# Kernel optimization log

Hardware: AMD Instinct MI355X
Metric: run time of the kernel (lower is better)

## Reference

```python
import jax, jax.numpy as jnp
import numpy as np

N = 100000      # nodes
E = 3200000     # edges (before self loops)
IN = 128        # in_channels
H = 8           # heads
C = 16          # out_channels per head
NEG_SLOPE = 0.2


def setup_inputs() -> dict:
    key = jax.random.key(0)
    k1, k2, k3, k4, k5, k6 = jax.random.split(key, 6)
    x = jax.random.normal(k1, (N, IN), dtype=jnp.float32)
    edge_index = jax.random.randint(k2, (2, E), 0, N, dtype=jnp.int32)
    # GATConv params: lin weight [IN, H*C], att_src/att_dst [H, C], bias [H*C]
    W = jax.random.normal(k3, (IN, H * C), dtype=jnp.float32) / np.float32(np.sqrt(IN))
    att_src = jax.random.normal(k4, (H, C), dtype=jnp.float32) / np.float32(np.sqrt(C))
    att_dst = jax.random.normal(k5, (H, C), dtype=jnp.float32) / np.float32(np.sqrt(C))
    bias = jax.random.normal(k6, (H * C,), dtype=jnp.float32) * 0.01
    return {"x": x, "edge_index": edge_index, "W": W,
            "att_src": att_src, "att_dst": att_dst, "bias": bias}


def reference(x, edge_index, W, att_src, att_dst, bias):
    n = x.shape[0]
    h = (x @ W).reshape(n, H, C)                      # [N, H, C]
    # add self loops (PyG default add_self_loops=True)
    loop = jnp.arange(n, dtype=edge_index.dtype)
    src = jnp.concatenate([edge_index[0], loop])      # [E+N] message sources j
    dst = jnp.concatenate([edge_index[1], loop])      # [E+N] targets i
    # per-node attention logits
    a_src = jnp.einsum('nhc,hc->nh', h, att_src)      # [N, H]
    a_dst = jnp.einsum('nhc,hc->nh', h, att_dst)      # [N, H]
    alpha = jax.nn.leaky_relu(a_src[src] + a_dst[dst], NEG_SLOPE)  # [E+N, H]
    # segment softmax over edges grouped by destination node
    amax = jax.lax.stop_gradient(jax.ops.segment_max(alpha, dst, num_segments=n))
    ex = jnp.exp(alpha - amax[dst])
    denom = jax.ops.segment_sum(ex, dst, num_segments=n)           # [N, H]
    w = ex / (denom[dst] + 1e-16)                                  # [E+N, H]
    msg = h[src] * w[:, :, None]                                   # [E+N, H, C]
    out = jax.ops.segment_sum(msg, dst, num_segments=n)            # [N, H, C]
    return out.reshape(n, H * C) + bias
```

## Files before the change

### kernel.cpp

```cpp
#include <hip/hip_runtime.h>
#include <hip/hip_bf16.h>

#define H 8
#define C 16
#define HC 128
#define NEG 0.2f
#define XS_S 132

#define BKT_SH 8
#define BKT_MSK 255
#define MAXB 1024
#define EPB 4096

__device__ __forceinline__ float lrelu(float x) { return fmaxf(x, NEG * x); }

__device__ __forceinline__ unsigned pack_bf16(float a, float b) {
    union { __hip_bfloat16 h; unsigned short u; } ua, ub;
    ua.h = __float2bfloat16(a);
    ub.h = __float2bfloat16(b);
    return (unsigned)ua.u | ((unsigned)ub.u << 16);
}
__device__ __forceinline__ float bf_lo(unsigned d) { return __uint_as_float(d << 16); }
__device__ __forceinline__ float bf_hi(unsigned d) { return __uint_as_float(d & 0xffff0000u); }

__global__ void __launch_bounds__(256) k1_gemm(const float* __restrict__ x,
                                               const float* __restrict__ W,
                                               const float* __restrict__ att_src,
                                               const float* __restrict__ att_dst,
                                               unsigned* __restrict__ h16,
                                               float* __restrict__ a_src,
                                               float* __restrict__ a_dst, int N) {
    __shared__ float xs[64 * XS_S];
    const int n0 = blockIdx.x * 64;
    const int t = threadIdx.x;
#pragma unroll
    for (int i = 0; i < 8; ++i) {
        int id = t + 256 * i;
        int r = id >> 5, kq = id & 31;
        int n = n0 + r;
        float4 v = (n < N) ? ((const float4*)x)[(size_t)n * 32 + kq]
                           : make_float4(0.f, 0.f, 0.f, 0.f);
        *(float4*)&xs[r * XS_S + kq * 4] = v;
    }
    __syncthreads();
    const int cg = t & 31;
    const int r0 = (t >> 5) * 8;
    float acc[8][4];
#pragma unroll
    for (int i = 0; i < 8; ++i)
#pragma unroll
        for (int j = 0; j < 4; ++j) acc[i][j] = 0.f;

#pragma unroll 4
    for (int k = 0; k < HC; ++k) {
        const float4 wv = ((const float4*)W)[k * 32 + cg];
        float wr[4] = {wv.x, wv.y, wv.z, wv.w};
#pragma unroll
        for (int i = 0; i < 8; ++i) {
            float xv = xs[(r0 + i) * XS_S + k];
#pragma unroll
            for (int j = 0; j < 4; ++j) acc[i][j] += xv * wr[j];
        }
    }
    const int fhd = cg >> 2;
    const int cq  = cg & 3;
#pragma unroll
    for (int i = 0; i < 8; ++i) {
        int n = n0 + r0 + i;
        if (n < N) {
            uint2 dv = make_uint2(pack_bf16(acc[i][0], acc[i][1]),
                                  pack_bf16(acc[i][2], acc[i][3]));
            *(uint2*)&h16[(size_t)n * 64 + cg * 2] = dv;
        }
        float ps = 0.f, pd = 0.f;
#pragma unroll
        for (int jj = 0; jj < 4; ++jj) {
            float hv = acc[i][jj];
            ps += hv * att_src[fhd * C + cq * 4 + jj];
            pd += hv * att_dst[fhd * C + cq * 4 + jj];
        }
        ps += __shfl_xor(ps, 1, 4); pd += __shfl_xor(pd, 1, 4);
        ps += __shfl_xor(ps, 2, 4); pd += __shfl_xor(pd, 2, 4);
        if (cq == 0 && n < N) {
            a_src[(unsigned)n * 8u + fhd] = ps;
            a_dst[(unsigned)n * 8u + fhd] = pd;
        }
    }
}


__global__ void __launch_bounds__(256) kh_bucket(const int* __restrict__ ei,
                                                 int* __restrict__ bcount,
                                                 int E, int B) {
    __shared__ int hist[MAXB];
    const int t = threadIdx.x;
    for (int i = t; i < B; i += 256) hist[i] = 0;
    __syncthreads();
    const int e0 = blockIdx.x * EPB;
    const int nE = min(EPB, E - e0);
    for (int i = t; i < nE; i += 256)
        atomicAdd(&hist[ei[E + e0 + i] >> BKT_SH], 1);
    __syncthreads();
    for (int i = t; i < B; i += 256)
        if (hist[i]) atomicAdd(&bcount[i], hist[i]);
}

__global__ void __launch_bounds__(1024) kscan_b(const int* __restrict__ bcount,
                                                int* __restrict__ bptr,
                                                int* __restrict__ gcursor,
                                                int* __restrict__ rowptr,
                                                int N, int B, int E) {
    __shared__ int s[MAXB];
    const int t = threadIdx.x;
    s[t] = (t < B) ? bcount[t] : 0;
    __syncthreads();
    for (int off = 1; off < MAXB; off <<= 1) {
        int v = (t >= off) ? s[t - off] : 0;
        __syncthreads();
        s[t] += v;
        __syncthreads();
    }
    if (t < B) {
        bptr[t + 1] = s[t];
        gcursor[t] = s[t] - bcount[t];
    }
    if (t == 0) { bptr[0] = 0; rowptr[N] = E; }
}

__global__ void __launch_bounds__(256) kb_bin(const int* __restrict__ ei,
                                              int* __restrict__ gcursor,
                                              unsigned* __restrict__ pairs,
                                              int E, int B) {
    __shared__ int hist[MAXB];
    __shared__ int lbase[MAXB];
    const int t = threadIdx.x;
    const int e0 = blockIdx.x * EPB;
    const int nE = min(EPB, E - e0);
    for (int i = t; i < B; i += 256) hist[i] = 0;
    __syncthreads();
    for (int i = t; i < nE; i += 256)
        atomicAdd(&hist[ei[E + e0 + i] >> BKT_SH], 1);
    __syncthreads();
    for (int i = t; i < B; i += 256) {
        int h = hist[i];
        if (h) lbase[i] = atomicAdd(&gcursor[i], h);
    }
    __syncthreads();
    for (int i = t; i < nE; i += 256) {
        int dst = ei[E + e0 + i];
        int src = ei[e0 + i];
        int b = dst >> BKT_SH;
        int pos = atomicAdd(&lbase[b], 1);
        pairs[pos] = (unsigned)src | ((unsigned)(dst & BKT_MSK) << 18);
    }
}

__global__ void __launch_bounds__(256) kb_final(const unsigned* __restrict__ pairs,
                                                const int* __restrict__ bptr,
                                                int* __restrict__ rowptr,
                                                int* __restrict__ col, int N) {
    __shared__ int cnt[256];
    __shared__ int incl[256];
    __shared__ int lcur[256];
    const int b = blockIdx.x;
    const int t = threadIdx.x;
    const int n0 = b << BKT_SH;
    const int jbeg = bptr[b], jend = bptr[b + 1];
    cnt[t] = 0;
    __syncthreads();
    for (int j = jbeg + t; j < jend; j += 256)
        atomicAdd(&cnt[pairs[j] >> 18], 1);
    __syncthreads();
    incl[t] = cnt[t];
    __syncthreads();
    for (int off = 1; off < 256; off <<= 1) {
        int v = (t >= off) ? incl[t - off] : 0;
        __syncthreads();
        incl[t] += v;
        __syncthreads();
    }
    const int base = jbeg + incl[t] - cnt[t];
    if (n0 + t < N) rowptr[n0 + t] = base;
    lcur[t] = base;
    __syncthreads();
    for (int j = jbeg + t; j < jend; j += 256) {
        unsigned v = pairs[j];
        int pos = atomicAdd(&lcur[v >> 18], 1);
        col[pos] = (int)(v & 0x3FFFF);
    }
}

__global__ void __launch_bounds__(256) k_pull(const int* __restrict__ rowptr,
                                              const int* __restrict__ col,
                                              const unsigned* __restrict__ h16,
                                              const float* __restrict__ a_src,
                                              const float* __restrict__ a_dst,
                                              const float* __restrict__ bias,
                                              float* __restrict__ out, int N) {
    const int node = blockIdx.x * 4 + (threadIdx.x >> 6);
    if (node >= N) return;
    const int t = threadIdx.x & 63;
    const int hd = t >> 3;
    const int hh = t & 7;
    const int bidx = hd * 4;

    const float adst_own = a_dst[(unsigned)node * 8u + (unsigned)hd];
    const float adst_hh  = a_dst[(unsigned)node * 8u + (unsigned)hh];
    const float wself = __expf(lrelu(a_src[(unsigned)node * 8u + (unsigned)hd] + adst_own));
    unsigned dself = h16[(unsigned)node * 64u + (unsigned)t];
    float a0 = bf_lo(dself) * wself, a1 = bf_hi(dself) * wself;
    float b0 = 0.f, b1 = 0.f, c0 = 0.f, c1 = 0.f, e0 = 0.f, e1 = 0.f;
    float sA = wself, sB = 0.f, sC = 0.f, sD = 0.f;

    const int beg = rowptr[node], end = rowptr[node + 1];
    int j = beg;
    for (; j + 8 <= end; j += 8) {
        int n0_ = col[j],     n1 = col[j + 1], n2 = col[j + 2], n3 = col[j + 3];
        int n4  = col[j + 4], n5 = col[j + 5], n6 = col[j + 6], n7 = col[j + 7];
        int nP = col[j + (t >> 3)];
        float wme = __expf(lrelu(a_src[(unsigned)nP * 8u + (unsigned)hh] + adst_hh));
        int wi = __float_as_int(wme);
        float w0 = __int_as_float(__builtin_amdgcn_ds_bpermute(bidx,       wi));
        float w1 = __int_as_float(__builtin_amdgcn_ds_bpermute(bidx + 32,  wi));
        float w2 = __int_as_float(__builtin_amdgcn_ds_bpermute(bidx + 64,  wi));
        float w3 = __int_as_float(__builtin_amdgcn_ds_bpermute(bidx + 96,  wi));
        float w4 = __int_as_float(__builtin_amdgcn_ds_bpermute(bidx + 128, wi));
        float w5 = __int_as_float(__builtin_amdgcn_ds_bpermute(bidx + 160, wi));
        float w6 = __int_as_float(__builtin_amdgcn_ds_bpermute(bidx + 192, wi));
        float w7 = __int_as_float(__builtin_amdgcn_ds_bpermute(bidx + 224, wi));
        unsigned d0 = h16[(unsigned)n0_ * 64u + (unsigned)t];
        unsigned d1 = h16[(unsigned)n1 * 64u + (unsigned)t];
        unsigned d2 = h16[(unsigned)n2 * 64u + (unsigned)t];
        unsigned d3 = h16[(unsigned)n3 * 64u + (unsigned)t];
        unsigned d4 = h16[(unsigned)n4 * 64u + (unsigned)t];
        unsigned d5 = h16[(unsigned)n5 * 64u + (unsigned)t];
        unsigned d6 = h16[(unsigned)n6 * 64u + (unsigned)t];
        unsigned d7 = h16[(unsigned)n7 * 64u + (unsigned)t];
        a0 += bf_lo(d0) * w0; a1 += bf_hi(d0) * w0; sA += w0;
        b0 += bf_lo(d1) * w1; b1 += bf_hi(d1) * w1; sB += w1;
        c0 += bf_lo(d2) * w2; c1 += bf_hi(d2) * w2; sC += w2;
        e0 += bf_lo(d3) * w3; e1 += bf_hi(d3) * w3; sD += w3;
        a0 += bf_lo(d4) * w4; a1 += bf_hi(d4) * w4; sA += w4;
        b0 += bf_lo(d5) * w5; b1 += bf_hi(d5) * w5; sB += w5;
        c0 += bf_lo(d6) * w6; c1 += bf_hi(d6) * w6; sC += w6;
        e0 += bf_lo(d7) * w7; e1 += bf_hi(d7) * w7; sD += w7;
    }
    if (j + 4 <= end) {
        int n0_ = col[j], n1 = col[j + 1], n2 = col[j + 2], n3 = col[j + 3];
        int nP = col[j + ((t >> 3) & 3)];
        float wme = __expf(lrelu(a_src[(unsigned)nP * 8u + (unsigned)hh] + adst_hh));
        int wi = __float_as_int(wme);
        float w0 = __int_as_float(__builtin_amdgcn_ds_bpermute(bidx,      wi));
        float w1 = __int_as_float(__builtin_amdgcn_ds_bpermute(bidx + 32, wi));
        float w2 = __int_as_float(__builtin_amdgcn_ds_bpermute(bidx + 64, wi));
        float w3 = __int_as_float(__builtin_amdgcn_ds_bpermute(bidx + 96, wi));
        unsigned d0 = h16[(unsigned)n0_ * 64u + (unsigned)t];
        unsigned d1 = h16[(unsigned)n1 * 64u + (unsigned)t];
        unsigned d2 = h16[(unsigned)n2 * 64u + (unsigned)t];
        unsigned d3 = h16[(unsigned)n3 * 64u + (unsigned)t];
        a0 += bf_lo(d0) * w0; a1 += bf_hi(d0) * w0; sA += w0;
        b0 += bf_lo(d1) * w1; b1 += bf_hi(d1) * w1; sB += w1;
        c0 += bf_lo(d2) * w2; c1 += bf_hi(d2) * w2; sC += w2;
        e0 += bf_lo(d3) * w3; e1 += bf_hi(d3) * w3; sD += w3;
        j += 4;
    }
    for (; j < end; ++j) {
        int nA = col[j];
        float wA = __expf(lrelu(a_src[(unsigned)nA * 8u + (unsigned)hd] + adst_own));
        unsigned dA = h16[(unsigned)nA * 64u + (unsigned)t];
        a0 += bf_lo(dA) * wA; a1 += bf_hi(dA) * wA; sA += wA;
    }
    const float s = sA + sB + sC + sD;
    const float inv = 1.f / (s + 1e-16f);
    const float acc0 = a0 + b0 + c0 + e0;
    const float acc1 = a1 + b1 + c1 + e1;
    const float2 bv = ((const float2*)bias)[t];
    float2 o;
    o.x = acc0 * inv + bv.x;
    o.y = acc1 * inv + bv.y;
    ((float2*)out)[(unsigned)node * 64u + (unsigned)t] = o;
}

extern "C" void kernel_launch(void* const* d_in, const int* in_sizes, int n_in,
                              void* d_out, int out_size, void* d_ws, size_t ws_size,
                              hipStream_t stream) {
    const float* x       = (const float*)d_in[0];
    const int*   ei      = (const int*)d_in[1];
    const float* W       = (const float*)d_in[2];
    const float* att_src = (const float*)d_in[3];
    const float* att_dst = (const float*)d_in[4];
    const float* bias    = (const float*)d_in[5];
    float* out = (float*)d_out;

    const int N = in_sizes[0] / HC;
    const int E = in_sizes[1] / 2;
    const int B = (N + BKT_MSK) >> BKT_SH;
    const int nbin = (E + EPB - 1) / EPB;

    unsigned* h16 = (unsigned*)d_ws;
    float* a_src  = (float*)(h16 + (size_t)N * 64);
    float* a_dst  = a_src + (size_t)N * H;
    int* bcount   = (int*)(a_dst + (size_t)N * H);
    int* bptr     = bcount + MAXB;
    int* gcursor  = bptr + (MAXB + 1);
    int* rowptr   = gcursor + MAXB;
    int* col      = rowptr + (N + 1);
    unsigned* pairs = (unsigned*)(col + E);

    (void)hipMemsetAsync(bcount, 0, MAXB * sizeof(int), stream);

    k1_gemm<<<(N + 63) / 64, 256, 0, stream>>>(x, W, att_src, att_dst,
                                               h16, a_src, a_dst, N);

    kh_bucket<<<nbin, 256, 0, stream>>>(ei, bcount, E, B);
    kscan_b<<<1, 1024, 0, stream>>>(bcount, bptr, gcursor, rowptr, N, B, E);
    kb_bin<<<nbin, 256, 0, stream>>>(ei, gcursor, pairs, E, B);
    kb_final<<<B, 256, 0, stream>>>(pairs, bptr, rowptr, col, N);

    k_pull<<<(N + 3) / 4, 256, 0, stream>>>(rowptr, col, h16, a_src,
                                            a_dst, bias, out, N);
}
```

Before: 437.6 us.

## Overlap CSR build with GEMM on side stream, vectorize binning, restructure pull

The CSR construction kernels (bucket histogram, scan, binning, final sort) now run on a separate non-blocking stream forked and joined with events, so they can overlap the feature GEMM. The bucket and bin kernels read edge indices as int4 when E is divisible by 4, cutting the number of load instructions. The pull kernel is reorganised so each half-wavefront handles alternating edges and loads 8-byte bf16 vectors per lane, then combines the halves with a shuffle and writes float4 outputs. This adds a static side stream and events, and in the remainder loop half the wave sits idle.

```diff
diff --git a/kernel.cpp b/kernel.cpp
--- a/kernel.cpp
+++ b/kernel.cpp
@@ -98,8 +98,22 @@
     __syncthreads();
     const int e0 = blockIdx.x * EPB;
     const int nE = min(EPB, E - e0);
-    for (int i = t; i < nE; i += 256)
-        atomicAdd(&hist[ei[E + e0 + i] >> BKT_SH], 1);
+    if ((E & 3) == 0) {
+        const int nE4 = nE >> 2;
+        const int4* d4p = (const int4*)(ei + E + e0);
+        for (int i = t; i < nE4; i += 256) {
+            int4 d = d4p[i];
+            atomicAdd(&hist[d.x >> BKT_SH], 1);
+            atomicAdd(&hist[d.y >> BKT_SH], 1);
+            atomicAdd(&hist[d.z >> BKT_SH], 1);
+            atomicAdd(&hist[d.w >> BKT_SH], 1);
+        }
+        for (int i = (nE4 << 2) + t; i < nE; i += 256)
+            atomicAdd(&hist[ei[E + e0 + i] >> BKT_SH], 1);
+    } else {
+        for (int i = t; i < nE; i += 256)
+            atomicAdd(&hist[ei[E + e0 + i] >> BKT_SH], 1);
+    }
     __syncthreads();
     for (int i = t; i < B; i += 256)
         if (hist[i]) atomicAdd(&bcount[i], hist[i]);
@@ -138,20 +152,55 @@
     const int nE = min(EPB, E - e0);
     for (int i = t; i < B; i += 256) hist[i] = 0;
     __syncthreads();
-    for (int i = t; i < nE; i += 256)
-        atomicAdd(&hist[ei[E + e0 + i] >> BKT_SH], 1);
+    const bool v4 = ((E & 3) == 0);
+    const int nE4 = v4 ? (nE >> 2) : 0;
+    const int4* d4p = (const int4*)(ei + E + e0);
+    const int4* s4p = (const int4*)(ei + e0);
+    if (v4) {
+        for (int i = t; i < nE4; i += 256) {
+            int4 d = d4p[i];
+            atomicAdd(&hist[d.x >> BKT_SH], 1);
+            atomicAdd(&hist[d.y >> BKT_SH], 1);
+            atomicAdd(&hist[d.z >> BKT_SH], 1);
+            atomicAdd(&hist[d.w >> BKT_SH], 1);
+        }
+        for (int i = (nE4 << 2) + t; i < nE; i += 256)
+            atomicAdd(&hist[ei[E + e0 + i] >> BKT_SH], 1);
+    } else {
+        for (int i = t; i < nE; i += 256)
+            atomicAdd(&hist[ei[E + e0 + i] >> BKT_SH], 1);
+    }
     __syncthreads();
     for (int i = t; i < B; i += 256) {
         int h = hist[i];
         if (h) lbase[i] = atomicAdd(&gcursor[i], h);
     }
     __syncthreads();
-    for (int i = t; i < nE; i += 256) {
-        int dst = ei[E + e0 + i];
-        int src = ei[e0 + i];
-        int b = dst >> BKT_SH;
-        int pos = atomicAdd(&lbase[b], 1);
-        pairs[pos] = (unsigned)src | ((unsigned)(dst & BKT_MSK) << 18);
+    if (v4) {
+        for (int i = t; i < nE4; i += 256) {
+            int4 d = d4p[i];
+            int4 sv = s4p[i];
+#pragma unroll
+            for (int q = 0; q < 4; ++q) {
+                int dst = (&d.x)[q], src = (&sv.x)[q];
+                int b = dst >> BKT_SH;
+                int pos = atomicAdd(&lbase[b], 1);
+                pairs[pos] = (unsigned)src | ((unsigned)(dst & BKT_MSK) << 18);
+            }
+        }
+        for (int i = (nE4 << 2) + t; i < nE; i += 256) {
+            int dst = ei[E + e0 + i], src = ei[e0 + i];
+            int b = dst >> BKT_SH;
+            int pos = atomicAdd(&lbase[b], 1);
+            pairs[pos] = (unsigned)src | ((unsigned)(dst & BKT_MSK) << 18);
+        }
+    } else {
+        for (int i = t; i < nE; i += 256) {
+            int dst = ei[E + e0 + i], src = ei[e0 + i];
+            int b = dst >> BKT_SH;
+            int pos = atomicAdd(&lbase[b], 1);
+            pairs[pos] = (unsigned)src | ((unsigned)(dst & BKT_MSK) << 18);
+        }
     }
 }
 
@@ -200,85 +249,61 @@
     const int node = blockIdx.x * 4 + (threadIdx.x >> 6);
     if (node >= N) return;
     const int t = threadIdx.x & 63;
-    const int hd = t >> 3;
-    const int hh = t & 7;
-    const int bidx = hd * 4;
-
-    const float adst_own = a_dst[(unsigned)node * 8u + (unsigned)hd];
-    const float adst_hh  = a_dst[(unsigned)node * 8u + (unsigned)hh];
-    const float wself = __expf(lrelu(a_src[(unsigned)node * 8u + (unsigned)hd] + adst_own));
-    unsigned dself = h16[(unsigned)node * 64u + (unsigned)t];
-    float a0 = bf_lo(dself) * wself, a1 = bf_hi(dself) * wself;
-    float b0 = 0.f, b1 = 0.f, c0 = 0.f, c1 = 0.f, e0 = 0.f, e1 = 0.f;
-    float sA = wself, sB = 0.f, sC = 0.f, sD = 0.f;
+    const int slot = t >> 5;
+    const int cc = t & 31;
+    const int hh2 = cc >> 2;
+    const int hw = t & 7;
+
+    const float adst_c = a_dst[(unsigned)node * 8u + (unsigned)hh2];
+    const float adst_w = a_dst[(unsigned)node * 8u + (unsigned)hw];
+
+    float f0 = 0.f, f1 = 0.f, f2 = 0.f, f3 = 0.f, s = 0.f;
+    if (slot == 0) {
+        const float wself = __expf(lrelu(a_src[(unsigned)node * 8u + (unsigned)hh2] + adst_c));
+        uint2 d = *(const uint2*)&h16[(unsigned)node * 64u + (unsigned)cc * 2u];
+        f0 = bf_lo(d.x) * wself; f1 = bf_hi(d.x) * wself;
+        f2 = bf_lo(d.y) * wself; f3 = bf_hi(d.y) * wself;
+        s = wself;
+    }
 
     const int beg = rowptr[node], end = rowptr[node + 1];
     int j = beg;
     for (; j + 8 <= end; j += 8) {
-        int n0_ = col[j],     n1 = col[j + 1], n2 = col[j + 2], n3 = col[j + 3];
-        int n4  = col[j + 4], n5 = col[j + 5], n6 = col[j + 6], n7 = col[j + 7];
         int nP = col[j + (t >> 3)];
-        float wme = __expf(lrelu(a_src[(unsigned)nP * 8u + (unsigned)hh] + adst_hh));
+        float wme = __expf(lrelu(a_src[(unsigned)nP * 8u + (unsigned)hw] + adst_w));
         int wi = __float_as_int(wme);
-        float w0 = __int_as_float(__builtin_amdgcn_ds_bpermute(bidx,       wi));
-        float w1 = __int_as_float(__builtin_amdgcn_ds_bpermute(bidx + 32,  wi));
-        float w2 = __int_as_float(__builtin_amdgcn_ds_bpermute(bidx + 64,  wi));
-        float w3 = __int_as_float(__builtin_amdgcn_ds_bpermute(bidx + 96,  wi));
-        float w4 = __int_as_float(__builtin_amdgcn_ds_bpermute(bidx + 128, wi));
-        float w5 = __int_as_float(__builtin_amdgcn_ds_bpermute(bidx + 160, wi));
-        float w6 = __int_as_float(__builtin_amdgcn_ds_bpermute(bidx + 192, wi));
-        float w7 = __int_as_float(__builtin_amdgcn_ds_bpermute(bidx + 224, wi));
-        unsigned d0 = h16[(unsigned)n0_ * 64u + (unsigned)t];
-        unsigned d1 = h16[(unsigned)n1 * 64u + (unsigned)t];
-        unsigned d2 = h16[(unsigned)n2 * 64u + (unsigned)t];
-        unsigned d3 = h16[(unsigned)n3 * 64u + (unsigned)t];
-        unsigned d4 = h16[(unsigned)n4 * 64u + (unsigned)t];
-        unsigned d5 = h16[(unsigned)n5 * 64u + (unsigned)t];
-        unsigned d6 = h16[(unsigned)n6 * 64u + (unsigned)t];
-        unsigned d7 = h16[(unsigned)n7 * 64u + (unsigned)t];
-        a0 += bf_lo(d0) * w0; a1 += bf_hi(d0) * w0; sA += w0;
-        b0 += bf_lo(d1) * w1; b1 += bf_hi(d1) * w1; sB += w1;
-        c0 += bf_lo(d2) * w2; c1 += bf_hi(d2) * w2; sC += w2;
-        e0 += bf_lo(d3) * w3; e1 += bf_hi(d3) * w3; sD += w3;
-        a0 += bf_lo(d4) * w4; a1 += bf_hi(d4) * w4; sA += w4;
-        b0 += bf_lo(d5) * w5; b1 += bf_hi(d5) * w5; sB += w5;
-        c0 += bf_lo(d6) * w6; c1 += bf_hi(d6) * w6; sC += w6;
-        e0 += bf_lo(d7) * w7; e1 += bf_hi(d7) * w7; sD += w7;
-    }
-    if (j + 4 <= end) {
-        int n0_ = col[j], n1 = col[j + 1], n2 = col[j + 2], n3 = col[j + 3];
-        int nP = col[j + ((t >> 3) & 3)];
-        float wme = __expf(lrelu(a_src[(unsigned)nP * 8u + (unsigned)hh] + adst_hh));
-        int wi = __float_as_int(wme);
-        float w0 = __int_as_float(__builtin_amdgcn_ds_bpermute(bidx,      wi));
-        float w1 = __int_as_float(__builtin_amdgcn_ds_bpermute(bidx + 32, wi));
-        float w2 = __int_as_float(__builtin_amdgcn_ds_bpermute(bidx + 64, wi));
-        float w3 = __int_as_float(__builtin_amdgcn_ds_bpermute(bidx + 96, wi));
-        unsigned d0 = h16[(unsigned)n0_ * 64u + (unsigned)t];
-        unsigned d1 = h16[(unsigned)n1 * 64u + (unsigned)t];
-        unsigned d2 = h16[(unsigned)n2 * 64u + (unsigned)t];
-        unsigned d3 = h16[(unsigned)n3 * 64u + (unsigned)t];
-        a0 += bf_lo(d0) * w0; a1 += bf_hi(d0) * w0; sA += w0;
-        b0 += bf_lo(d1) * w1; b1 += bf_hi(d1) * w1; sB += w1;
-        c0 += bf_lo(d2) * w2; c1 += bf_hi(d2) * w2; sC += w2;
-        e0 += bf_lo(d3) * w3; e1 += bf_hi(d3) * w3; sD += w3;
-        j += 4;
+#pragma unroll
+        for (int k = 0; k < 4; ++k) {
+            const int e = slot + 2 * k;
+            int ne = col[j + e];
+            float w = __int_as_float(
+                __builtin_amdgcn_ds_bpermute((e * 8 + hh2) * 4, wi));
+            uint2 d = *(const uint2*)&h16[(unsigned)ne * 64u + (unsigned)cc * 2u];
+            f0 += bf_lo(d.x) * w; f1 += bf_hi(d.x) * w;
+            f2 += bf_lo(d.y) * w; f3 += bf_hi(d.y) * w;
+            s += w;
+        }
     }
     for (; j < end; ++j) {
-        int nA = col[j];
-        float wA = __expf(lrelu(a_src[(unsigned)nA * 8u + (unsigned)hd] + adst_own));
-        unsigned dA = h16[(unsigned)nA * 64u + (unsigned)t];
-        a0 += bf_lo(dA) * wA; a1 += bf_hi(dA) * wA; sA += wA;
-    }
-    const float s = sA + sB + sC + sD;
-    const float inv = 1.f / (s + 1e-16f);
-    const float acc0 = a0 + b0 + c0 + e0;
-    const float acc1 = a1 + b1 + c1 + e1;
-    const float2 bv = ((const float2*)bias)[t];
-    float2 o;
-    o.x = acc0 * inv + bv.x;
-    o.y = acc1 * inv + bv.y;
-    ((float2*)out)[(unsigned)node * 64u + (unsigned)t] = o;
+        if (slot == 0) {
+            int ne = col[j];
+            float w = __expf(lrelu(a_src[(unsigned)ne * 8u + (unsigned)hh2] + adst_c));
+            uint2 d = *(const uint2*)&h16[(unsigned)ne * 64u + (unsigned)cc * 2u];
+            f0 += bf_lo(d.x) * w; f1 += bf_hi(d.x) * w;
+            f2 += bf_lo(d.y) * w; f3 += bf_hi(d.y) * w;
+            s += w;
+        }
+    }
+    f0 += __shfl_xor(f0, 32); f1 += __shfl_xor(f1, 32);
+    f2 += __shfl_xor(f2, 32); f3 += __shfl_xor(f3, 32);
+    s  += __shfl_xor(s, 32);
+    if (slot == 0) {
+        const float inv = 1.f / (s + 1e-16f);
+        const float4 bv = ((const float4*)bias)[cc];
+        float4 o = make_float4(f0 * inv + bv.x, f1 * inv + bv.y,
+                               f2 * inv + bv.z, f3 * inv + bv.w);
+        ((float4*)out)[(unsigned)node * 32u + (unsigned)cc] = o;
+    }
 }
 
 extern "C" void kernel_launch(void* const* d_in, const int* in_sizes, int n_in,
@@ -307,15 +332,32 @@
     int* col      = rowptr + (N + 1);
     unsigned* pairs = (unsigned*)(col + E);
 
-    (void)hipMemsetAsync(bcount, 0, MAXB * sizeof(int), stream);
+    static hipStream_t s_side = nullptr;
+    static hipEvent_t ev_fork = nullptr, ev_join = nullptr;
+    if (s_side == nullptr) {
+        (void)hipStreamCreateWithFlags(&s_side, hipStreamNonBlocking);
+        (void)hipEventCreateWithFlags(&ev_fork, hipEventDisableTiming);
+        (void)hipEventCreateWithFlags(&ev_join, hipEventDisableTiming);
+    }
+    const bool fork = (s_side != nullptr && ev_fork != nullptr && ev_join != nullptr);
+    hipStream_t sb = fork ? s_side : stream;
+
+    if (fork) {
+        (void)hipEventRecord(ev_fork, stream);
+        (void)hipStreamWaitEvent(sb, ev_fork, 0);
+    }
+
+    (void)hipMemsetAsync(bcount, 0, MAXB * sizeof(int), sb);
+    kh_bucket<<<nbin, 256, 0, sb>>>(ei, bcount, E, B);
+    kscan_b<<<1, 1024, 0, sb>>>(bcount, bptr, gcursor, rowptr, N, B, E);
+    kb_bin<<<nbin, 256, 0, sb>>>(ei, gcursor, pairs, E, B);
+    kb_final<<<B, 256, 0, sb>>>(pairs, bptr, rowptr, col, N);
+    if (fork) (void)hipEventRecord(ev_join, sb);
 
     k1_gemm<<<(N + 63) / 64, 256, 0, stream>>>(x, W, att_src, att_dst,
                                                h16, a_src, a_dst, N);
 
-    kh_bucket<<<nbin, 256, 0, stream>>>(ei, bcount, E, B);
-    kscan_b<<<1, 1024, 0, stream>>>(bcount, bptr, gcursor, rowptr, N, B, E);
-    kb_bin<<<nbin, 256, 0, stream>>>(ei, gcursor, pairs, E, B);
-    kb_final<<<B, 256, 0, stream>>>(pairs, bptr, rowptr, col, N);
+    if (fork) (void)hipStreamWaitEvent(stream, ev_join, 0);
 
     k_pull<<<(N + 3) / 4, 256, 0, stream>>>(rowptr, col, h16, a_src,
                                             a_dst, bias, out, N);
```

New measurement: 436.5 us. Within noise of the previous version (-0.3%).
